# Performance work log

Measured on AMD Instinct MI355X. Metric: run time of the kernel, lower is better.

## Reference

```python
import jax, jax.numpy as jnp
import numpy as np

B, C, D = 512, 50000, 256
N_LOADED = 40000


def setup_inputs() -> dict:
    key = jax.random.key(0)
    k1, k2, k3, k4 = jax.random.split(key, 4)
    visual_feats = jax.random.normal(k1, (B, D), dtype=jnp.float32)
    text_feats = jax.random.normal(k2, (C, D), dtype=jnp.float32)
    # sparse multi-hot labels; force class 0 positive for every row so the
    # positive set (intersected with loaded ids) is never empty
    batch_label = (jax.random.uniform(k3, (B, C)) < 0.02).astype(jnp.int32)
    batch_label = batch_label.at[:, 0].set(1)
    # distinct loaded class ids; force id 0 to be loaded
    ids = jax.random.permutation(k4, C)[:N_LOADED].astype(jnp.int32)
    ids = jnp.sort(ids).at[0].set(0)
    return {
        "visual_feats": visual_feats,
        "text_feats": text_feats,
        "batch_label": batch_label,
        "class_ids_loaded": ids,
        "d_space": D,
    }


def reference(visual_feats, text_feats, batch_label, class_ids_loaded, d_space):
    num_classes = text_feats.shape[0]
    # membership mask for loaded class ids (the set() intersection in torch)
    loaded = jnp.zeros((num_classes,), dtype=bool).at[class_ids_loaded].set(True)

    # cosine similarity; note: torch adds 1e-6 eps only to text-feature norms
    v = visual_feats / jnp.linalg.norm(visual_feats, axis=1, keepdims=True)
    t = text_feats / (1e-6 + jnp.linalg.norm(text_feats, axis=1, keepdims=True))
    S = v @ t.T  # [B, C]

    pos = (batch_label != 0) & loaded[None, :]  # ragged positive sets, as mask
    neg = (batch_label == 0) & loaded[None, :]  # ragged negative sets, as mask

    # denominator: sum of exp(sim) over negatives, per row
    denom = jnp.sum(jnp.where(neg, jnp.exp(S), 0.0), axis=1)  # [B]
    n_pos = jnp.sum(pos, axis=1).astype(S.dtype)  # [B]

    # per-row loss: mean over positives of -log(exp(s_p)/denom) = log(denom)-s_p
    per_row = jnp.sum(jnp.where(pos, jnp.log(denom)[:, None] - S, 0.0), axis=1) / n_pos
    return jnp.mean(per_row).reshape(1)
```

## Files before the change

### kernel.cpp

```cpp
#include <hip/hip_runtime.h>
#include <math.h>

#define D_DIM 256
#define TM 128
#define TN 128
#define BK 32
#define NBP 392

typedef __attribute__((ext_vector_type(8))) short short8;
typedef __attribute__((ext_vector_type(4))) float floatx4;
typedef unsigned long long u64;

__device__ __forceinline__ unsigned short f2bf(float f) {
    unsigned int u = __float_as_uint(f);
    u += 0x7FFFu + ((u >> 16) & 1u);
    return (unsigned short)(u >> 16);
}

__device__ __forceinline__ void gload16(const void* g, void* lds) {
    __builtin_amdgcn_global_load_lds(
        (const __attribute__((address_space(1))) unsigned int*)g,
        (__attribute__((address_space(3))) unsigned int*)lds, 16, 0, 0);
}

__global__ void prep(const float* __restrict__ V, const float* __restrict__ T,
                     const int* __restrict__ ids, u64* __restrict__ loadedmask,
                     unsigned short* __restrict__ Vb, unsigned short* __restrict__ Tb,
                     int B, int C, int n_loaded, int WPR) {
    int gtid = blockIdx.x * blockDim.x + threadIdx.x;
    if (gtid < WPR) {
        int base = gtid << 6;
        int lo = 0, hi = n_loaded;
        while (lo < hi) { int mid = (lo + hi) >> 1; if (ids[mid] < base) lo = mid + 1; else hi = mid; }
        u64 m = 0;
        for (int i = lo; i < n_loaded; ++i) {
            int v = ids[i]; if (v >= base + 64) break;
            m |= 1ull << (v - base);
        }
        loadedmask[gtid] = m;
    }
    int wave = gtid >> 6;
    int lane = threadIdx.x & 63;
    if (wave >= B + C) return;
    bool isV = wave < B;
    const float* src = isV ? (V + (size_t)wave * D_DIM)
                           : (T + (size_t)(wave - B) * D_DIM);
    float4 x = ((const float4*)src)[lane];
    float ss = x.x * x.x + x.y * x.y + x.z * x.z + x.w * x.w;
    #pragma unroll
    for (int off = 32; off > 0; off >>= 1) ss += __shfl_xor(ss, off);
    float nrm = sqrtf(ss);
    float s = isV ? (1.0f / nrm) : (1.0f / (1e-6f + nrm));
    ushort4 o;
    o.x = f2bf(x.x * s); o.y = f2bf(x.y * s);
    o.z = f2bf(x.z * s); o.w = f2bf(x.w * s);
    unsigned short* dst = isV ? (Vb + (size_t)wave * D_DIM)
                              : (Tb + (size_t)(wave - B) * D_DIM);
    ((ushort4*)dst)[lane] = o;
}

__global__ void compress(const int* __restrict__ label, const u64* __restrict__ loadedmask,
                         u64* __restrict__ posmask, int C, int WPR) {
    int row  = blockIdx.y;
    int wir  = blockIdx.x * 4 + (threadIdx.x >> 6);
    int lane = threadIdx.x & 63;
    int w0   = wir * 16;
    if (w0 >= WPR) return;
    const int* lp = label + (size_t)row * C;
    int lab[16];
    #pragma unroll
    for (int j = 0; j < 16; ++j) {
        int wc  = w0 + j;
        int col = (wc << 6) | lane;
        lab[j] = (wc < WPR && col < C) ? lp[col] : 0;
    }
    #pragma unroll
    for (int j = 0; j < 16; ++j) {
        int wc = w0 + j;
        if (wc < WPR) {
            u64 posw = __ballot(lab[j] != 0) & loadedmask[wc];
            if (lane == 0) posmask[(size_t)row * WPR + wc] = posw;
        }
    }
}

__global__ __launch_bounds__(256) void gemm_fused(
    const unsigned short* __restrict__ Vb, const unsigned short* __restrict__ Tb,
    const u64* __restrict__ posmask, const u64* __restrict__ loadedmask,
    float* __restrict__ denomP, float* __restrict__ posP, int C, int WPR) {
    __shared__ unsigned short As[TM * BK];
    __shared__ unsigned short Bs[TN * BK];
    __shared__ float sDen[TM], sPos[TM];

    const int tid  = threadIdx.x;
    const int lane = tid & 63;
    const int w    = tid >> 6;
    const int m0 = blockIdx.x * TM;
    const int n0 = blockIdx.y * TN;

    if (tid < TM) { sDen[tid] = 0.f; sPos[tid] = 0.f; }

    const int sra = lane >> 2;
    const int kc  = (lane & 3) * 8;
    int ga  = m0 + w * 32 + sra;
    int gb0 = n0 + w * 32 + sra;
    int gb1 = gb0 + 16;
    if (gb0 >= C) gb0 = C - 1;
    if (gb1 >= C) gb1 = C - 1;
    const unsigned short* gA0 = Vb + (size_t)ga * D_DIM + kc;
    const unsigned short* gA1 = gA0 + (size_t)16 * D_DIM;
    const unsigned short* gB0 = Tb + (size_t)gb0 * D_DIM + kc;
    const unsigned short* gB1 = Tb + (size_t)gb1 * D_DIM + kc;
    unsigned short* lA0 = &As[w * 32 * BK];
    unsigned short* lA1 = lA0 + 16 * BK;
    unsigned short* lB0 = &Bs[w * 32 * BK];
    unsigned short* lB1 = lB0 + 16 * BK;

    const int wm = (w >> 1) * 64;
    const int wn = (w & 1) * 64;
    const int fr = lane & 15;
    const int quad = lane >> 4;

    floatx4 acc[4][4];
    #pragma unroll
    for (int mi = 0; mi < 4; mi++)
        #pragma unroll
        for (int ni = 0; ni < 4; ni++) acc[mi][ni] = (floatx4)0.f;

    #pragma unroll
    for (int kt = 0; kt < D_DIM / BK; ++kt) {
        if (kt) __syncthreads();
        const int kb = kt * BK;
        gload16(gA0 + kb, lA0);
        gload16(gA1 + kb, lA1);
        gload16(gB0 + kb, lB0);
        gload16(gB1 + kb, lB1);
        __syncthreads();
        short8 af[4], bf[4];
        #pragma unroll
        for (int mi = 0; mi < 4; mi++)
            af[mi] = *(const short8*)&As[(wm + mi * 16 + fr) * BK + quad * 8];
        #pragma unroll
        for (int ni = 0; ni < 4; ni++)
            bf[ni] = *(const short8*)&Bs[(wn + ni * 16 + fr) * BK + quad * 8];
        #pragma unroll
        for (int mi = 0; mi < 4; mi++)
            #pragma unroll
            for (int ni = 0; ni < 4; ni++)
                acc[mi][ni] = __builtin_amdgcn_mfma_f32_16x16x32_bf16(
                    af[mi], bf[ni], acc[mi][ni], 0, 0, 0);
    }

    const int wcol = (n0 + wn) >> 6;
    const u64 loadedw = loadedmask[wcol];
    #pragma unroll
    for (int mi = 0; mi < 4; mi++) {
        #pragma unroll
        for (int i = 0; i < 4; i++) {
            const int mloc = wm + mi * 16 + quad * 4 + i;
            const u64 posw = posmask[(size_t)(m0 + mloc) * WPR + wcol];
            const u64 negw = loadedw & ~posw;
            float den = 0.f, pos = 0.f;
            #pragma unroll
            for (int ni = 0; ni < 4; ni++) {
                const float s = acc[mi][ni][i];
                const int bit = ni * 16 + fr;
                if ((negw >> bit) & 1) den += __expf(s);
                if ((posw >> bit) & 1) pos += s;
            }
            #pragma unroll
            for (int off = 8; off >= 1; off >>= 1) {
                den += __shfl_xor(den, off);
                pos += __shfl_xor(pos, off);
            }
            if (fr == 0) {
                if (den != 0.f) atomicAdd(&sDen[mloc], den);
                if (pos != 0.f) atomicAdd(&sPos[mloc], pos);
            }
        }
    }
    __syncthreads();
    if (tid < TM) {
        denomP[(size_t)(m0 + tid) * NBP + blockIdx.y] = sDen[tid];
        posP[(size_t)(m0 + tid) * NBP + blockIdx.y]   = sPos[tid];
    }
}

__global__ void reduce_rows(const float* __restrict__ denomP, const float* __restrict__ posP,
                            const u64* __restrict__ posmask, float* __restrict__ pr,
                            int B, int NB, int WPR) {
    int row  = blockIdx.x * 4 + (threadIdx.x >> 6);
    int lane = threadIdx.x & 63;
    if (row >= B) return;
    float den = 0.f, pos = 0.f;
    for (int bn = lane; bn < NB; bn += 64) {
        den += denomP[(size_t)row * NBP + bn];
        pos += posP[(size_t)row * NBP + bn];
    }
    int cnt = 0;
    for (int j = lane; j < WPR; j += 64)
        cnt += __popcll(posmask[(size_t)row * WPR + j]);
    #pragma unroll
    for (int off = 32; off > 0; off >>= 1) {
        den += __shfl_xor(den, off);
        pos += __shfl_xor(pos, off);
        cnt += __shfl_xor(cnt, off);
    }
    if (lane == 0) pr[row] = logf(den) - pos / (float)cnt;
}

__global__ void final_mean(const float* __restrict__ pr, float* __restrict__ out, int B) {
    __shared__ float red[512];
    int tid = threadIdx.x;
    red[tid] = (tid < B) ? pr[tid] : 0.f;
    __syncthreads();
    for (int s = 256; s > 0; s >>= 1) {
        if (tid < s) red[tid] += red[tid + s];
        __syncthreads();
    }
    if (tid == 0) out[0] = red[0] / (float)B;
}

extern "C" void kernel_launch(void* const* d_in, const int* in_sizes, int n_in,
                              void* d_out, int out_size, void* d_ws, size_t ws_size,
                              hipStream_t stream) {
    const float* V     = (const float*)d_in[0];
    const float* T     = (const float*)d_in[1];
    const int*   label = (const int*)d_in[2];
    const int*   ids   = (const int*)d_in[3];
    int B = in_sizes[0] / D_DIM;
    int C = in_sizes[1] / D_DIM;
    int n_loaded = in_sizes[3];
    int WPR = (C + 63) >> 6;
    int NB  = (C + TN - 1) / TN;

    char* ws = (char*)d_ws;
    float* pr      = (float*)(ws + 0);
    u64*   loadedmask = (u64*)(ws + 2048);
    u64*   posmask    = (u64*)(ws + 8320);
    unsigned short* Vb = (unsigned short*)(ws + 3211392);
    unsigned short* Tb = (unsigned short*)(ws + 3473536);
    float* denomP  = (float*)(ws + 29073536);
    float* posP    = (float*)(ws + 29876352);

    int threads_needed = (B + C) * 64;
    prep<<<(threads_needed + 255) / 256, 256, 0, stream>>>(
        V, T, ids, loadedmask, Vb, Tb, B, C, n_loaded, WPR);

    int wavesPerRow = (WPR + 15) / 16;
    dim3 cgrid((wavesPerRow + 3) / 4, B);
    compress<<<cgrid, 256, 0, stream>>>(label, loadedmask, posmask, C, WPR);

    dim3 grid(B / TM, NB);
    gemm_fused<<<grid, 256, 0, stream>>>(Vb, Tb, posmask, loadedmask,
                                         denomP, posP, C, WPR);

    reduce_rows<<<(B + 3) / 4, 256, 0, stream>>>(denomP, posP, posmask, pr, B, NB, WPR);

    final_mean<<<1, 512, 0, stream>>>(pr, (float*)d_out, B);
}
```

Baseline: 305.2 us.

## Fuse label compression into prep, vectorize label reads, fold final mean into reduce

Merges the label-to-bitmask compression into the prep kernel so it no longer waits on the loaded-id mask, since the loaded-mask AND is now applied later in the GEMM epilogue and in the row reduction. Labels are read as int4 vectors and packed with shuffles instead of per-element ballots. The separate final-mean kernel is removed; reduce_rows accumulates per-block sums with atomics and the last block writes the output. This drops two kernel launches and lets label streaming overlap normalization, at the cost of non-deterministic float atomic summation order.

```diff
diff --git a/kernel.cpp b/kernel.cpp
--- a/kernel.cpp
+++ b/kernel.cpp
@@ -6,6 +6,8 @@
 #define TN 128
 #define BK 32
 #define NBP 392
+#define CBPR 7
+#define CBLKS (CBPR * 512)
 
 typedef __attribute__((ext_vector_type(8))) short short8;
 typedef __attribute__((ext_vector_type(4))) float floatx4;
@@ -23,13 +25,59 @@
         (__attribute__((address_space(3))) unsigned int*)lds, 16, 0, 0);
 }
 
-__global__ void prep(const float* __restrict__ V, const float* __restrict__ T,
-                     const int* __restrict__ ids, u64* __restrict__ loadedmask,
-                     unsigned short* __restrict__ Vb, unsigned short* __restrict__ Tb,
-                     int B, int C, int n_loaded, int WPR) {
-    int gtid = blockIdx.x * blockDim.x + threadIdx.x;
-    if (gtid < WPR) {
-        int base = gtid << 6;
+__global__ __launch_bounds__(256) void prep_compress(
+    const float* __restrict__ V, const float* __restrict__ T,
+    const int* __restrict__ label, const int* __restrict__ ids,
+    u64* __restrict__ loadedmask, u64* __restrict__ posmask,
+    unsigned short* __restrict__ Vb, unsigned short* __restrict__ Tb,
+    float* __restrict__ gaccum, unsigned int* __restrict__ gcount,
+    int B, int C, int n_loaded, int WPR) {
+    const int bid = blockIdx.x;
+    const int tid = threadIdx.x;
+    const int lane = tid & 63;
+
+    if (bid < CBLKS) {
+        int row = bid / CBPR;
+        int sub = bid - row * CBPR;
+        int wl  = tid >> 6;
+        int w0col = (sub * 4 + wl) * 2048;
+        if (w0col >= C) return;
+        const int* lp = label + (size_t)row * C;
+        int4 lo[4], hi[4];
+        #pragma unroll
+        for (int r = 0; r < 4; ++r) {
+            int c0 = w0col + r * 512 + lane * 8;
+            if (c0 < C) {
+                lo[r] = *(const int4*)(lp + c0);
+                hi[r] = *(const int4*)(lp + c0 + 4);
+            } else {
+                lo[r] = make_int4(0, 0, 0, 0);
+                hi[r] = make_int4(0, 0, 0, 0);
+            }
+        }
+        #pragma unroll
+        for (int r = 0; r < 4; ++r) {
+            unsigned int by =
+                (lo[r].x ? 1u : 0u) | (lo[r].y ? 2u : 0u) |
+                (lo[r].z ? 4u : 0u) | (lo[r].w ? 8u : 0u) |
+                (hi[r].x ? 16u : 0u) | (hi[r].y ? 32u : 0u) |
+                (hi[r].z ? 64u : 0u) | (hi[r].w ? 128u : 0u);
+            u64 wv = (u64)by << (8 * (lane & 7));
+            wv |= __shfl_xor(wv, 1);
+            wv |= __shfl_xor(wv, 2);
+            wv |= __shfl_xor(wv, 4);
+            if ((lane & 7) == 0) {
+                int wc = ((w0col + r * 512) >> 6) + (lane >> 3);
+                if (wc < WPR) posmask[(size_t)row * WPR + wc] = wv;
+            }
+        }
+        return;
+    }
+
+    int ptid = (bid - CBLKS) * 256 + tid;
+    if (ptid == 0) { *gcount = 0u; *gaccum = 0.f; }
+    if (ptid < WPR) {
+        int base = ptid << 6;
         int lo = 0, hi = n_loaded;
         while (lo < hi) { int mid = (lo + hi) >> 1; if (ids[mid] < base) lo = mid + 1; else hi = mid; }
         u64 m = 0;
@@ -37,10 +85,9 @@
             int v = ids[i]; if (v >= base + 64) break;
             m |= 1ull << (v - base);
         }
-        loadedmask[gtid] = m;
-    }
-    int wave = gtid >> 6;
-    int lane = threadIdx.x & 63;
+        loadedmask[ptid] = m;
+    }
+    int wave = ptid >> 6;
     if (wave >= B + C) return;
     bool isV = wave < B;
     const float* src = isV ? (V + (size_t)wave * D_DIM)
@@ -57,31 +104,6 @@
     unsigned short* dst = isV ? (Vb + (size_t)wave * D_DIM)
                               : (Tb + (size_t)(wave - B) * D_DIM);
     ((ushort4*)dst)[lane] = o;
-}
-
-__global__ void compress(const int* __restrict__ label, const u64* __restrict__ loadedmask,
-                         u64* __restrict__ posmask, int C, int WPR) {
-    int row  = blockIdx.y;
-    int wir  = blockIdx.x * 4 + (threadIdx.x >> 6);
-    int lane = threadIdx.x & 63;
-    int w0   = wir * 16;
-    if (w0 >= WPR) return;
-    const int* lp = label + (size_t)row * C;
-    int lab[16];
-    #pragma unroll
-    for (int j = 0; j < 16; ++j) {
-        int wc  = w0 + j;
-        int col = (wc << 6) | lane;
-        lab[j] = (wc < WPR && col < C) ? lp[col] : 0;
-    }
-    #pragma unroll
-    for (int j = 0; j < 16; ++j) {
-        int wc = w0 + j;
-        if (wc < WPR) {
-            u64 posw = __ballot(lab[j] != 0) & loadedmask[wc];
-            if (lane == 0) posmask[(size_t)row * WPR + wc] = posw;
-        }
-    }
 }
 
 __global__ __launch_bounds__(256) void gemm_fused(
@@ -158,8 +180,9 @@
         #pragma unroll
         for (int i = 0; i < 4; i++) {
             const int mloc = wm + mi * 16 + quad * 4 + i;
-            const u64 posw = posmask[(size_t)(m0 + mloc) * WPR + wcol];
-            const u64 negw = loadedw & ~posw;
+            const u64 praw = posmask[(size_t)(m0 + mloc) * WPR + wcol];
+            const u64 posw = praw & loadedw;
+            const u64 negw = loadedw & ~praw;
             float den = 0.f, pos = 0.f;
             #pragma unroll
             for (int ni = 0; ni < 4; ni++) {
@@ -187,38 +210,41 @@
 }
 
 __global__ void reduce_rows(const float* __restrict__ denomP, const float* __restrict__ posP,
-                            const u64* __restrict__ posmask, float* __restrict__ pr,
-                            int B, int NB, int WPR) {
-    int row  = blockIdx.x * 4 + (threadIdx.x >> 6);
+                            const u64* __restrict__ posmask, const u64* __restrict__ loadedmask,
+                            float* __restrict__ gaccum, unsigned int* __restrict__ gcount,
+                            float* __restrict__ out, int B, int NB, int WPR) {
+    __shared__ float bsum[4];
+    int wv   = threadIdx.x >> 6;
+    int row  = blockIdx.x * 4 + wv;
     int lane = threadIdx.x & 63;
-    if (row >= B) return;
     float den = 0.f, pos = 0.f;
-    for (int bn = lane; bn < NB; bn += 64) {
-        den += denomP[(size_t)row * NBP + bn];
-        pos += posP[(size_t)row * NBP + bn];
-    }
     int cnt = 0;
-    for (int j = lane; j < WPR; j += 64)
-        cnt += __popcll(posmask[(size_t)row * WPR + j]);
-    #pragma unroll
-    for (int off = 32; off > 0; off >>= 1) {
-        den += __shfl_xor(den, off);
-        pos += __shfl_xor(pos, off);
-        cnt += __shfl_xor(cnt, off);
-    }
-    if (lane == 0) pr[row] = logf(den) - pos / (float)cnt;
-}
-
-__global__ void final_mean(const float* __restrict__ pr, float* __restrict__ out, int B) {
-    __shared__ float red[512];
-    int tid = threadIdx.x;
-    red[tid] = (tid < B) ? pr[tid] : 0.f;
+    if (row < B) {
+        for (int bn = lane; bn < NB; bn += 64) {
+            den += denomP[(size_t)row * NBP + bn];
+            pos += posP[(size_t)row * NBP + bn];
+        }
+        for (int j = lane; j < WPR; j += 64)
+            cnt += __popcll(posmask[(size_t)row * WPR + j] & loadedmask[j]);
+        #pragma unroll
+        for (int off = 32; off > 0; off >>= 1) {
+            den += __shfl_xor(den, off);
+            pos += __shfl_xor(pos, off);
+            cnt += __shfl_xor(cnt, off);
+        }
+    }
+    if (lane == 0) bsum[wv] = (row < B) ? (logf(den) - pos / (float)cnt) : 0.f;
     __syncthreads();
-    for (int s = 256; s > 0; s >>= 1) {
-        if (tid < s) red[tid] += red[tid + s];
-        __syncthreads();
-    }
-    if (tid == 0) out[0] = red[0] / (float)B;
+    if (threadIdx.x == 0) {
+        float s = bsum[0] + bsum[1] + bsum[2] + bsum[3];
+        atomicAdd(gaccum, s);
+        __threadfence();
+        unsigned int old = atomicAdd(gcount, 1u);
+        if (old == gridDim.x - 1) {
+            float tot = atomicAdd(gaccum, 0.0f);
+            out[0] = tot / (float)B;
+        }
+    }
 }
 
 extern "C" void kernel_launch(void* const* d_in, const int* in_sizes, int n_in,
@@ -235,7 +261,8 @@
     int NB  = (C + TN - 1) / TN;
 
     char* ws = (char*)d_ws;
-    float* pr      = (float*)(ws + 0);
+    float*        gaccum = (float*)(ws + 0);
+    unsigned int* gcount = (unsigned int*)(ws + 8);
     u64*   loadedmask = (u64*)(ws + 2048);
     u64*   posmask    = (u64*)(ws + 8320);
     unsigned short* Vb = (unsigned short*)(ws + 3211392);
@@ -243,19 +270,15 @@
     float* denomP  = (float*)(ws + 29073536);
     float* posP    = (float*)(ws + 29876352);
 
-    int threads_needed = (B + C) * 64;
-    prep<<<(threads_needed + 255) / 256, 256, 0, stream>>>(
-        V, T, ids, loadedmask, Vb, Tb, B, C, n_loaded, WPR);
-
-    int wavesPerRow = (WPR + 15) / 16;
-    dim3 cgrid((wavesPerRow + 3) / 4, B);
-    compress<<<cgrid, 256, 0, stream>>>(label, loadedmask, posmask, C, WPR);
+    int prep_blocks = ((B + C) * 64 + 255) / 256;
+    prep_compress<<<CBLKS + prep_blocks, 256, 0, stream>>>(
+        V, T, label, ids, loadedmask, posmask, Vb, Tb, gaccum, gcount,
+        B, C, n_loaded, WPR);
 
     dim3 grid(B / TM, NB);
     gemm_fused<<<grid, 256, 0, stream>>>(Vb, Tb, posmask, loadedmask,
                                          denomP, posP, C, WPR);
 
-    reduce_rows<<<(B + 3) / 4, 256, 0, stream>>>(denomP, posP, posmask, pr, B, NB, WPR);
-
-    final_mean<<<1, 512, 0, stream>>>(pr, (float*)d_out, B);
-}
+    reduce_rows<<<(B + 3) / 4, 256, 0, stream>>>(denomP, posP, posmask, loadedmask,
+                                                 gaccum, gcount, (float*)d_out, B, NB, WPR);
+}
```

Result: faster. 263.3 us (-13.7%).
